# Kernel tuning notes

Measured on AMD Instinct MI355X. Metric: run time of the kernel, lower is better.

## Reference

```python
import jax, jax.numpy as jnp
import numpy as np

N = 200000   # nodes
R = 4        # relations
E = 1000000  # edges per relation
B = 1024     # graphs in batch


def _graph_conv(h, s, d, ew, W, b):
    """DGL GraphConv, norm='both', optional edge_weight. h:[N,F_in] -> [N,F_out]."""
    n = h.shape[0]
    ones = jnp.ones(s.shape[0], dtype=h.dtype)
    out_deg = jnp.clip(jax.ops.segment_sum(ones, s, num_segments=n), 1.0)
    in_deg = jnp.clip(jax.ops.segment_sum(ones, d, num_segments=n), 1.0)
    hs = h * jax.lax.rsqrt(out_deg)[:, None]          # src-side norm
    m = hs[s]                                         # gather: [E, F_in]
    if ew is not None:
        m = m * ew[:, None]
    agg = jax.ops.segment_sum(m, d, num_segments=n)   # scatter-sum: [N, F_in]
    rst = agg * jax.lax.rsqrt(in_deg)[:, None]        # dst-side norm
    return rst @ W + b


def _hetero_layer(h, src, dst, ew, W, b):
    out = None
    for r in range(R):
        ewr = None if ew is None else ew[r]
        o = _graph_conv(h, src[r], dst[r], ewr, W[r], b[r])
        out = o if out is None else out + o
    return out


def setup_inputs() -> dict:
    key = jax.random.key(0)
    ks = jax.random.split(key, 10)
    feat = jax.random.normal(ks[0], (N, 2), dtype=jnp.float32)
    src = jax.random.randint(ks[1], (R, E), 0, N, dtype=jnp.int32)
    dst = jax.random.randint(ks[2], (R, E), 0, N, dtype=jnp.int32)
    ew = jax.random.uniform(ks[3], (R, E), dtype=jnp.float32)
    graph_ids = jnp.sort(jax.random.randint(ks[4], (N,), 0, B, dtype=jnp.int32))
    W1 = jax.random.normal(ks[5], (R, 2, 16), dtype=jnp.float32) * 0.5
    b1 = jnp.zeros((R, 16), dtype=jnp.float32)
    W2 = jax.random.normal(ks[6], (R, 16, 16), dtype=jnp.float32) * 0.25
    b2 = jnp.zeros((R, 16), dtype=jnp.float32)
    Wc = jax.random.normal(ks[7], (16, 2), dtype=jnp.float32) * 0.25
    bc = jnp.zeros((2,), dtype=jnp.float32)
    return {"feat": feat, "src": src, "dst": dst, "ew": ew,
            "graph_ids": graph_ids, "W1": W1, "b1": b1,
            "W2": W2, "b2": b2, "Wc": Wc, "bc": bc}


def reference(feat, src, dst, ew, graph_ids, W1, b1, W2, b2, Wc, bc):
    # layer 1: per-relation weighted GraphConv, summed over relations
    h = _hetero_layer(feat, src, dst, ew, W1, b1)
    h = jax.nn.relu(h)
    # layer 2: no edge weights (kwargs not forwarded in original code)
    h = _hetero_layer(h, src, dst, None, W2, b2)
    # mean_nodes per graph in the batch
    sums = jax.ops.segment_sum(h, graph_ids, num_segments=B)          # [B,16]
    cnts = jax.ops.segment_sum(jnp.ones((N,), h.dtype), graph_ids, num_segments=B)
    hg = sums / jnp.clip(cnts, 1.0)[:, None]
    return hg @ Wc + bc                                               # [B,2]
```

## Files before the change

### kernel.cpp

```cpp
#include <hip/hip_runtime.h>
#include <hip/hip_fp16.h>

#define NN 200000
#define RR 4
#define EE 1000000
#define BB 1024
#define RN (RR*NN)

#define BSH 7
#define BSZ 128
#define NB 1563
#define RK (RR*NB)
#define EPB 16384
#define SBT 1024
#define BPR ((EE + EPB - 1) / EPB)
#define GSLOTS 32
#define CAPB 1024

#define SRC_OF(u)  (((u) >> 7) & 0x3FFFF)
#define DL_OF(u)   ((int)((u) & 127))
#define DEG_OF(u)  ((u) >> 25)

#define OFF_POOL   0
#define OFF_CNT    (OFF_POOL + BB*16)
#define OFF_GCUR_S (OFF_CNT + BB)
#define OFF_GCUR_D (OFF_GCUR_S + RK)
#define ZERO_UNITS (OFF_GCUR_D + RK)
#define OFF_DEGB   ZERO_UNITS
#define OFF_INVI   (OFF_DEGB + RN/4)
#define OFF_RW16   (OFF_INVI + RN)
#define OFF_AGG1   (OFF_RW16 + RN/2)
#define OFF_H1H    (OFF_AGG1 + RN*2)
#define OFF_KW_    (OFF_H1H + NN*8)
#define OFF_KW     (OFF_KW_ + (OFF_KW_ & 1))


__global__ __launch_bounds__(SBT) void k_scat_src(const int* __restrict__ src,
                                                  int* __restrict__ gcur_s,
                                                  unsigned char* __restrict__ srcbin) {
  __shared__ int cnt[NB];
  __shared__ int base[NB];
  __shared__ int lcur[NB];
  int t = threadIdx.x, r = blockIdx.y, c0 = blockIdx.x * EPB;
  for (int i = t; i < NB; i += SBT) cnt[i] = 0;
  __syncthreads();
  for (int i = t; i < EPB; i += SBT) {
    int e = c0 + i;
    if (e < EE) atomicAdd(&cnt[src[r * EE + e] >> BSH], 1);
  }
  __syncthreads();
  for (int b = t; b < NB; b += SBT) {
    int v = cnt[b];
    base[b] = v ? atomicAdd(&gcur_s[r * NB + b], v) : 0;
    lcur[b] = 0;
  }
  __syncthreads();
  for (int i = t; i < EPB; i += SBT) {
    int e = c0 + i;
    if (e < EE) {
      int s = src[r * EE + e];
      int b = s >> BSH;
      int off = base[b] + atomicAdd(&lcur[b], 1);
      if (off < CAPB)
        srcbin[(size_t)(r * NB + b) * CAPB + off] = (unsigned char)(s & (BSZ - 1));
    }
  }
}

__global__ __launch_bounds__(128) void k_deg(const unsigned char* __restrict__ srcbin,
                                             const int* __restrict__ gcur_s,
                                             unsigned char* __restrict__ degb) {
  __shared__ int cnt[BSZ];
  int t = threadIdx.x, b = blockIdx.x, r = blockIdx.y;
  cnt[t] = 0;
  __syncthreads();
  int k = r * NB + b;
  size_t st = (size_t)k * CAPB;
  int m = min(gcur_s[k], CAPB);
  for (int e = t; e < m; e += 128) atomicAdd(&cnt[srcbin[st + e]], 1);
  __syncthreads();
  int n = (b << BSH) + t;
  if (n < NN) degb[r * NN + n] = (unsigned char)min(max(cnt[t], 1), 63);
}

__global__ __launch_bounds__(SBT) void k_scat_dst(const int* __restrict__ src,
                                                  const int* __restrict__ dst,
                                                  const float* __restrict__ ew,
                                                  const unsigned char* __restrict__ degb,
                                                  int* __restrict__ gcur_d,
                                                  long long* __restrict__ kw) {
  __shared__ int cnt[NB];
  __shared__ int base[NB];
  __shared__ int lcur[NB];
  int t = threadIdx.x, r = blockIdx.y, c0 = blockIdx.x * EPB;
  for (int i = t; i < NB; i += SBT) cnt[i] = 0;
  __syncthreads();
  for (int i = t; i < EPB; i += SBT) {
    int e = c0 + i;
    if (e < EE) atomicAdd(&cnt[dst[r * EE + e] >> BSH], 1);
  }
  __syncthreads();
  for (int b = t; b < NB; b += SBT) {
    int v = cnt[b];
    base[b] = v ? atomicAdd(&gcur_d[r * NB + b], v) : 0;
    lcur[b] = 0;
  }
  __syncthreads();
  for (int i = t; i < EPB; i += SBT) {
    int e = c0 + i;
    if (e < EE) {
      int idx = r * EE + e;
      int d = dst[idx], s = src[idx];
      int b = d >> BSH;
      int off = base[b] + atomicAdd(&lcur[b], 1);
      if (off < CAPB) {
        unsigned dg = degb[r * NN + s];
        float io = rsqrtf((float)dg);
        unsigned short w1h = __half_as_ushort(__float2half_rn(ew[idx] * io));
        unsigned low = (unsigned)(d & (BSZ - 1)) | ((unsigned)s << 7) | (dg << 25);
        kw[(size_t)(r * NB + b) * CAPB + off] =
            (long long)(((unsigned long long)w1h << 32) | low);
      }
    }
  }
}

__global__ __launch_bounds__(256) void k_l1a(long long* __restrict__ kw,
                                             const int* __restrict__ gcur_d,
                                             const float* __restrict__ feat,
                                             float* __restrict__ invi,
                                             unsigned short* __restrict__ rw16,
                                             float* __restrict__ agg1) {
  __shared__ long long bufraw[CAPB];
  __shared__ long long bufsort[CAPB];
  __shared__ int cnt[BSZ];
  __shared__ int scn[BSZ];
  __shared__ int cur[BSZ];
  __shared__ float la[BSZ * 3];
  int t = threadIdx.x, b = blockIdx.x, r = blockIdx.y;
  int n0 = b << BSH;
  int k = r * NB + b;
  size_t st = (size_t)k * CAPB;
  int m = min(gcur_d[k], CAPB);
  if (t < BSZ) { cnt[t] = 0; la[t * 3] = 0.f; la[t * 3 + 1] = 0.f; }
  for (int i = t; i < m; i += 256) bufraw[i] = kw[st + i];
  __syncthreads();
  for (int i = t; i < m; i += 256)
    atomicAdd(&cnt[DL_OF((unsigned)bufraw[i])], 1);
  __syncthreads();
  if (t < BSZ) scn[t] = cnt[t];
  __syncthreads();
  for (int off = 1; off < BSZ; off <<= 1) {
    int v = (t < BSZ && t >= off) ? scn[t - off] : 0;
    __syncthreads();
    if (t < BSZ) scn[t] += v;
    __syncthreads();
  }
  if (t < BSZ) {
    int excl = scn[t] - cnt[t];
    cur[t] = excl;
    int n = n0 + t;
    if (n < NN) {
      invi[r * NN + n] = rsqrtf((float)max(cnt[t], 1));
      rw16[r * NN + n] = (unsigned short)excl;
    }
  }
  __syncthreads();
  for (int i = t; i < m; i += 256) {
    long long kv = bufraw[i];
    bufsort[atomicAdd(&cur[DL_OF((unsigned)kv)], 1)] = kv;
  }
  __syncthreads();
  {
    unsigned* up = (unsigned*)kw + 2 * st + CAPB;
    for (int i = t; i < m; i += 256) up[i] = (unsigned)bufsort[i];
  }
  {
    int f = t & 1, grp = t >> 1;
    int seg = (m + BSZ - 1) >> 7;
    int e = grp * seg;
    int e1 = min(e + seg, m);
    float acc = 0.f;
    int dlprev = -1, dlfirst = -1;
    for (; e < e1; e++) {
      long long kv = bufsort[e];
      unsigned low = (unsigned)kv;
      int dl = DL_OF(low);
      int s = SRC_OF(low);
      float w = __half2float(__ushort_as_half((unsigned short)((unsigned long long)kv >> 32)));
      float fv = feat[s * 2 + f];
      if (dl != dlprev) {
        if (dlprev < 0) dlfirst = dl;
        else if (dlprev == dlfirst) atomicAdd(&la[dlprev * 3 + f], acc);
        else la[dlprev * 3 + f] = acc;
        acc = 0.f; dlprev = dl;
      }
      acc += fv * w;
    }
    if (dlprev >= 0) atomicAdd(&la[dlprev * 3 + f], acc);
  }
  __syncthreads();
  if (t < BSZ) {
    int n = n0 + t;
    if (n < NN)
      ((float2*)agg1)[r * NN + n] = make_float2(la[t * 3], la[t * 3 + 1]);
  }
}

__device__ __forceinline__ unsigned pack2h(float a, float b) {
  __half2 h = __floats2half2_rn(a, b);
  return *reinterpret_cast<unsigned*>(&h);
}

__global__ __launch_bounds__(256) void k_l1b(const float* __restrict__ agg1,
                                             const float* __restrict__ invi,
                                             const float* __restrict__ W1,
                                             const float* __restrict__ b1,
                                             __half* __restrict__ h1h) {
  __shared__ float sW[RR * 2 * 16];
  __shared__ float sb[16];
  int t = threadIdx.x, b = blockIdx.x;
  if (t < RR * 2 * 16) sW[t] = W1[t];
  if (t < 16) {
    float s = 0.f;
    for (int r = 0; r < RR; r++) s += b1[r * 16 + t];
    sb[t] = s;
  }
  __syncthreads();
  int n = b * 256 + t;
  if (n >= NN) return;
  float acc[16];
#pragma unroll
  for (int j = 0; j < 16; j++) acc[j] = sb[j];
#pragma unroll
  for (int r = 0; r < RR; r++) {
    float iv = invi[r * NN + n];
    float2 a = ((const float2*)agg1)[r * NN + n];
    float a0 = a.x * iv, a1 = a.y * iv;
#pragma unroll
    for (int j = 0; j < 16; j++)
      acc[j] += a0 * sW[(r * 2 + 0) * 16 + j] + a1 * sW[(r * 2 + 1) * 16 + j];
  }
#pragma unroll
  for (int j = 0; j < 16; j++) acc[j] = fmaxf(acc[j], 0.f);
  uint4 u0, u1;
  u0.x = pack2h(acc[0], acc[1]);  u0.y = pack2h(acc[2], acc[3]);
  u0.z = pack2h(acc[4], acc[5]);  u0.w = pack2h(acc[6], acc[7]);
  u1.x = pack2h(acc[8], acc[9]);  u1.y = pack2h(acc[10], acc[11]);
  u1.z = pack2h(acc[12], acc[13]); u1.w = pack2h(acc[14], acc[15]);
  uint4* o = (uint4*)(h1h + (size_t)n * 16);
  o[0] = u0; o[1] = u1;
}

__device__ __forceinline__ void acc8(float* acc, uint4 u, float w) {
  float2 p;
  p = __half22float2(*(__half2*)&u.x); acc[0] += p.x * w; acc[1] += p.y * w;
  p = __half22float2(*(__half2*)&u.y); acc[2] += p.x * w; acc[3] += p.y * w;
  p = __half22float2(*(__half2*)&u.z); acc[4] += p.x * w; acc[5] += p.y * w;
  p = __half22float2(*(__half2*)&u.w); acc[6] += p.x * w; acc[7] += p.y * w;
}

__global__ __launch_bounds__(256) void k_l2(const long long* __restrict__ kw,
                                            const int* __restrict__ gcur_d,
                                            const unsigned short* __restrict__ rw16,
                                            const __half* __restrict__ h1h,
                                            const float* __restrict__ invi,
                                            const float* __restrict__ W2,
                                            const int* __restrict__ gid,
                                            float* __restrict__ pool,
                                            float* __restrict__ cnt) {
  __shared__ float agg[BSZ * 17];
  __shared__ float sW[16 * 16];
  __shared__ int   sg[BSZ];
  __shared__ unsigned short srw[BSZ + 1];
  __shared__ float gslot[GSLOTS * 16];
  __shared__ int   cslot[GSLOTS];
  __shared__ int   present[GSLOTS];
  int t = threadIdx.x, b = blockIdx.x, r = blockIdx.y;
  int n0 = b << BSH;
  int k = r * NB + b;
  int m = min(gcur_d[k], CAPB);
  sW[t] = W2[r * 256 + t];
  if (t < GSLOTS) { cslot[t] = 0; present[t] = 0; }
  for (int i = t; i < GSLOTS * 16; i += 256) gslot[i] = 0.f;
  if (t < BSZ) {
    int n = n0 + t;
    srw[t] = (n < NN) ? rw16[r * NN + n] : (unsigned short)m;
  }
  if (t == BSZ) srw[BSZ] = (unsigned short)m;
  __syncthreads();
  const uint4* h4p = (const uint4*)h1h;
  const unsigned* rb = (const unsigned*)kw + 2 * (size_t)k * CAPB + CAPB;
  int f8 = t & 1, g = t >> 1;
  int e = srw[g], en = srw[g + 1];
  float acc[8];
#pragma unroll
  for (int j = 0; j < 8; j++) acc[j] = 0.f;
  for (; e + 3 < en; e += 4) {
    unsigned r0 = rb[e], r1 = rb[e + 1], r2 = rb[e + 2], r3 = rb[e + 3];
    uint4 u0 = h4p[(size_t)SRC_OF(r0) * 2 + f8];
    uint4 u1 = h4p[(size_t)SRC_OF(r1) * 2 + f8];
    uint4 u2 = h4p[(size_t)SRC_OF(r2) * 2 + f8];
    uint4 u3 = h4p[(size_t)SRC_OF(r3) * 2 + f8];
    acc8(acc, u0, rsqrtf((float)DEG_OF(r0)));
    acc8(acc, u1, rsqrtf((float)DEG_OF(r1)));
    acc8(acc, u2, rsqrtf((float)DEG_OF(r2)));
    acc8(acc, u3, rsqrtf((float)DEG_OF(r3)));
  }
  for (; e < en; e++) {
    unsigned rr = rb[e];
    uint4 u = h4p[(size_t)SRC_OF(rr) * 2 + f8];
    acc8(acc, u, rsqrtf((float)DEG_OF(rr)));
  }
#pragma unroll
  for (int j = 0; j < 8; j++) agg[g * 17 + 8 * f8 + j] = acc[j];
  __syncthreads();
  int n = n0 + t;
  int g0 = gid[n0];
  bool valid = (t < BSZ) && (n < NN);
  float out[16];
#pragma unroll
  for (int j = 0; j < 16; j++) out[j] = 0.f;
  if (valid) {
    float iv = invi[r * NN + n];
#pragma unroll
    for (int kk = 0; kk < 16; kk++) {
      float a = agg[t * 17 + kk] * iv;
#pragma unroll
      for (int j = 0; j < 16; j++) out[j] += a * sW[kk * 16 + j];
    }
  }
  __syncthreads();
  if (t < BSZ) {
    sg[t] = valid ? (gid[n] - g0) : -1;
#pragma unroll
    for (int j = 0; j < 16; j++) agg[t * 17 + j] = out[j];
  }
  __syncthreads();
  {
    int f = t & 15, i0 = t >> 4;
    for (int i = i0; i < BSZ; i += 16) {
      int gsN = sg[i];
      if (gsN < 0) continue;
      float v = agg[i * 17 + f];
      if (gsN < GSLOTS) {
        atomicAdd(&gslot[gsN * 16 + f], v);
        if (f == 0) {
          present[gsN] = 1;
          if (r == 0) atomicAdd(&cslot[gsN], 1);
        }
      } else {
        atomicAdd(&pool[(g0 + gsN) * 16 + f], v);
        if (f == 0 && r == 0) atomicAdd(&cnt[g0 + gsN], 1.0f);
      }
    }
  }
  __syncthreads();
  if (t < GSLOTS * 16) {
    int gsN = t >> 4, f = t & 15;
    if (present[gsN]) atomicAdd(&pool[(g0 + gsN) * 16 + f], gslot[t]);
  }
  if (r == 0 && t < GSLOTS && cslot[t] > 0)
    atomicAdd(&cnt[g0 + t], (float)cslot[t]);
}

__global__ __launch_bounds__(256) void k_final(const float* __restrict__ pool,
                                               const float* __restrict__ cnt,
                                               const float* __restrict__ b2,
                                               const float* __restrict__ Wc,
                                               const float* __restrict__ bc,
                                               float* __restrict__ out) {
  int b = blockIdx.x * 256 + threadIdx.x;
  if (b >= BB) return;
  float c = cnt[b];
  float inv = 1.0f / fmaxf(c, 1.0f);
  float o0 = bc[0], o1 = bc[1];
#pragma unroll
  for (int j = 0; j < 16; j++) {
    float sb = 0.f;
    for (int r = 0; r < RR; r++) sb += b2[r * 16 + j];
    float v = (pool[b * 16 + j] + c * sb) * inv;
    o0 += v * Wc[j * 2 + 0];
    o1 += v * Wc[j * 2 + 1];
  }
  out[b * 2 + 0] = o0;
  out[b * 2 + 1] = o1;
}

extern "C" void kernel_launch(void* const* d_in, const int* in_sizes, int n_in,
                              void* d_out, int out_size, void* d_ws, size_t ws_size,
                              hipStream_t stream) {
  const float* feat = (const float*)d_in[0];
  const int*   src  = (const int*)d_in[1];
  const int*   dst  = (const int*)d_in[2];
  const float* ew   = (const float*)d_in[3];
  const int*   gid  = (const int*)d_in[4];
  const float* W1   = (const float*)d_in[5];
  const float* b1   = (const float*)d_in[6];
  const float* W2   = (const float*)d_in[7];
  const float* b2   = (const float*)d_in[8];
  const float* Wc   = (const float*)d_in[9];
  const float* bc   = (const float*)d_in[10];

  char* ws = (char*)d_ws;
  float* pool   = (float*)(ws + (size_t)OFF_POOL   * 4);
  float* cnt    = (float*)(ws + (size_t)OFF_CNT    * 4);
  int*   gcur_s = (int*)  (ws + (size_t)OFF_GCUR_S * 4);
  int*   gcur_d = (int*)  (ws + (size_t)OFF_GCUR_D * 4);
  unsigned char*  degb = (unsigned char*) (ws + (size_t)OFF_DEGB * 4);
  float* invi   = (float*)(ws + (size_t)OFF_INVI   * 4);
  unsigned short* rw16 = (unsigned short*)(ws + (size_t)OFF_RW16 * 4);
  float* agg1   = (float*)(ws + (size_t)OFF_AGG1   * 4);
  __half* h1h   = (__half*)(ws + (size_t)OFF_H1H   * 4);
  long long* kw = (long long*)(ws + (size_t)OFF_KW * 4);

  hipMemsetAsync(d_ws, 0, (size_t)ZERO_UNITS * 4, stream);

  k_scat_src<<<dim3(BPR, RR), SBT, 0, stream>>>(src, gcur_s, (unsigned char*)kw);
  k_deg     <<<dim3(NB, RR), 128, 0, stream>>>((const unsigned char*)kw, gcur_s, degb);
  k_scat_dst<<<dim3(BPR, RR), SBT, 0, stream>>>(src, dst, ew, degb, gcur_d, kw);
  k_l1a     <<<dim3(NB, RR), 256, 0, stream>>>(kw, gcur_d, feat, invi, rw16, agg1);
  k_l1b     <<<(NN + 255) / 256, 256, 0, stream>>>(agg1, invi, W1, b1, h1h);
  k_l2      <<<dim3(NB, RR), 256, 0, stream>>>(kw, gcur_d, rw16, h1h, invi, W2, gid, pool, cnt);
  k_final   <<<(BB + 255) / 256, 256, 0, stream>>>(pool, cnt, b2, Wc, bc, (float*)d_out);
}
```

Baseline: 338.4 us.

## Replace per-128-node dst binning with two-pass superbin scatter and sort

The destination scatter now bins edges into 2048-node superbins (98 per relation) instead of 1563 small bins, and a new k_sortB kernel counting-sorts each superbin by node into compact src/weight arrays. k_l1a and k_l2 then read their edge ranges from these sorted arrays using per-node offsets. This cuts the number of global atomic bin cursors and shared-memory histogram work in the scatter pass, and gives more coalesced bin writes. The cost is an extra kernel and an extra pass over the edge data. Superbin capacity is fixed, and offsets are stored as 16-bit values, so overflow is possible on skewed inputs.

Result: slower. 370.7 us (+9.5%).

```diff
diff --git a/kernel.cpp b/kernel.cpp
--- a/kernel.cpp
+++ b/kernel.cpp
@@ -11,9 +11,12 @@
 #define BSZ 128
 #define NB 1563
 #define RK (RR*NB)
+#define SBSH 11
+#define NSB 98
+#define CAPSB 11264
 #define EPB 16384
+#define BPR ((EE + EPB - 1) / EPB)
 #define SBT 1024
-#define BPR ((EE + EPB - 1) / EPB)
 #define GSLOTS 32
 #define CAPB 1024
 
@@ -21,18 +24,19 @@
 #define DL_OF(u)   ((int)((u) & 127))
 #define DEG_OF(u)  ((u) >> 25)
 
-#define OFF_POOL   0
-#define OFF_CNT    (OFF_POOL + BB*16)
-#define OFF_GCUR_S (OFF_CNT + BB)
-#define OFF_GCUR_D (OFF_GCUR_S + RK)
-#define ZERO_UNITS (OFF_GCUR_D + RK)
-#define OFF_DEGB   ZERO_UNITS
-#define OFF_INVI   (OFF_DEGB + RN/4)
-#define OFF_RW16   (OFF_INVI + RN)
-#define OFF_AGG1   (OFF_RW16 + RN/2)
-#define OFF_H1H    (OFF_AGG1 + RN*2)
-#define OFF_KW_    (OFF_H1H + NN*8)
-#define OFF_KW     (OFF_KW_ + (OFF_KW_ & 1))
+#define OFF_POOL    0
+#define OFF_CNT     (OFF_POOL + BB*16)
+#define OFF_GCUR_S  (OFF_CNT + BB)
+#define OFF_GCUR_SB (OFF_GCUR_S + RK)
+#define ZERO_UNITS  (OFF_GCUR_SB + RR*NSB)
+#define OFF_DEGB    ZERO_UNITS
+#define OFF_INVI    (OFF_DEGB + RN/4)
+#define OFF_RW16    (OFF_INVI + RN)
+#define OFF_AGG1    (OFF_RW16 + RN/2)
+#define OFF_H1H     (OFF_AGG1 + RN*2)
+#define OFF_SBB     (OFF_H1H + NN*8)
+#define OFF_CS      (OFF_SBB + RR*NSB*CAPSB*2)
+#define OFF_W1S     (OFF_CS + RR*NSB*CAPSB)
 
 
 __global__ __launch_bounds__(SBT) void k_scat_src(const int* __restrict__ src,
@@ -83,27 +87,27 @@
   if (n < NN) degb[r * NN + n] = (unsigned char)min(max(cnt[t], 1), 63);
 }
 
-__global__ __launch_bounds__(SBT) void k_scat_dst(const int* __restrict__ src,
+__global__ __launch_bounds__(SBT) void k_scat_sbA(const int* __restrict__ src,
                                                   const int* __restrict__ dst,
                                                   const float* __restrict__ ew,
                                                   const unsigned char* __restrict__ degb,
-                                                  int* __restrict__ gcur_d,
-                                                  long long* __restrict__ kw) {
-  __shared__ int cnt[NB];
-  __shared__ int base[NB];
-  __shared__ int lcur[NB];
+                                                  int* __restrict__ gcur_sb,
+                                                  long long* __restrict__ sbb) {
+  __shared__ int cnt[NSB];
+  __shared__ int base[NSB];
+  __shared__ int lcur[NSB];
   int t = threadIdx.x, r = blockIdx.y, c0 = blockIdx.x * EPB;
-  for (int i = t; i < NB; i += SBT) cnt[i] = 0;
+  if (t < NSB) cnt[t] = 0;
   __syncthreads();
   for (int i = t; i < EPB; i += SBT) {
     int e = c0 + i;
-    if (e < EE) atomicAdd(&cnt[dst[r * EE + e] >> BSH], 1);
-  }
-  __syncthreads();
-  for (int b = t; b < NB; b += SBT) {
-    int v = cnt[b];
-    base[b] = v ? atomicAdd(&gcur_d[r * NB + b], v) : 0;
-    lcur[b] = 0;
+    if (e < EE) atomicAdd(&cnt[dst[r * EE + e] >> SBSH], 1);
+  }
+  __syncthreads();
+  if (t < NSB) {
+    int v = cnt[t];
+    base[t] = v ? atomicAdd(&gcur_sb[r * NSB + t], v) : 0;
+    lcur[t] = 0;
   }
   __syncthreads();
   for (int i = t; i < EPB; i += SBT) {
@@ -111,83 +115,108 @@
     if (e < EE) {
       int idx = r * EE + e;
       int d = dst[idx], s = src[idx];
-      int b = d >> BSH;
-      int off = base[b] + atomicAdd(&lcur[b], 1);
-      if (off < CAPB) {
+      int sb = d >> SBSH;
+      int off = base[sb] + atomicAdd(&lcur[sb], 1);
+      if (off < CAPSB) {
         unsigned dg = degb[r * NN + s];
         float io = rsqrtf((float)dg);
         unsigned short w1h = __half_as_ushort(__float2half_rn(ew[idx] * io));
+        unsigned bl = (unsigned)(d >> BSH) & 15;
         unsigned low = (unsigned)(d & (BSZ - 1)) | ((unsigned)s << 7) | (dg << 25);
-        kw[(size_t)(r * NB + b) * CAPB + off] =
-            (long long)(((unsigned long long)w1h << 32) | low);
+        unsigned high = (unsigned)w1h | (bl << 16);
+        sbb[(size_t)(r * NSB + sb) * CAPSB + off] =
+            (long long)(((unsigned long long)high << 32) | low);
       }
     }
   }
 }
 
-__global__ __launch_bounds__(256) void k_l1a(long long* __restrict__ kw,
-                                             const int* __restrict__ gcur_d,
+__global__ __launch_bounds__(1024) void k_sortB(const long long* __restrict__ sbb,
+                                                const int* __restrict__ gcur_sb,
+                                                float* __restrict__ invi,
+                                                unsigned short* __restrict__ rw16,
+                                                unsigned* __restrict__ cs,
+                                                unsigned short* __restrict__ w1s) {
+  __shared__ int cnt2[2048];
+  __shared__ int cur2[2048];
+  __shared__ int ssum[1024];
+  int t = threadIdx.x, sb = blockIdx.x, r = blockIdx.y;
+  int ksb = r * NSB + sb;
+  size_t sbase = (size_t)ksb * CAPSB;
+  int m = min(gcur_sb[ksb], CAPSB);
+  cnt2[t] = 0; cnt2[t + 1024] = 0;
+  __syncthreads();
+  for (int i = t; i < m; i += 1024) {
+    long long kv = sbb[sbase + i];
+    int node = (((int)(kv >> 48) & 15) << BSH) | ((int)kv & (BSZ - 1));
+    atomicAdd(&cnt2[node], 1);
+  }
+  __syncthreads();
+  int a0 = cnt2[2 * t], a1 = cnt2[2 * t + 1];
+  ssum[t] = a0 + a1;
+  __syncthreads();
+  for (int off = 1; off < 1024; off <<= 1) {
+    int v = (t >= off) ? ssum[t - off] : 0;
+    __syncthreads();
+    ssum[t] += v;
+    __syncthreads();
+  }
+  int e0 = (t > 0) ? ssum[t - 1] : 0;
+  int e1 = e0 + a0;
+  cur2[2 * t] = e0;
+  cur2[2 * t + 1] = e1;
+  {
+    int nbase = (sb << SBSH) + 2 * t;
+    if (nbase < NN) {
+      rw16[r * NN + nbase] = (unsigned short)e0;
+      invi[r * NN + nbase] = rsqrtf((float)max(a0, 1));
+    }
+    if (nbase + 1 < NN) {
+      rw16[r * NN + nbase + 1] = (unsigned short)e1;
+      invi[r * NN + nbase + 1] = rsqrtf((float)max(a1, 1));
+    }
+  }
+  __syncthreads();
+  for (int i = t; i < m; i += 1024) {
+    long long kv = sbb[sbase + i];
+    unsigned low = (unsigned)kv;
+    int node = (((int)(kv >> 48) & 15) << BSH) | (int)(low & (BSZ - 1));
+    int pos = atomicAdd(&cur2[node], 1);
+    cs[sbase + pos] = low;
+    w1s[sbase + pos] = (unsigned short)((unsigned long long)kv >> 32);
+  }
+}
+
+__global__ __launch_bounds__(256) void k_l1a(const unsigned* __restrict__ cs,
+                                             const unsigned short* __restrict__ w1s,
+                                             const int* __restrict__ gcur_sb,
+                                             const unsigned short* __restrict__ rw16,
                                              const float* __restrict__ feat,
-                                             float* __restrict__ invi,
-                                             unsigned short* __restrict__ rw16,
                                              float* __restrict__ agg1) {
-  __shared__ long long bufraw[CAPB];
-  __shared__ long long bufsort[CAPB];
-  __shared__ int cnt[BSZ];
-  __shared__ int scn[BSZ];
-  __shared__ int cur[BSZ];
   __shared__ float la[BSZ * 3];
   int t = threadIdx.x, b = blockIdx.x, r = blockIdx.y;
   int n0 = b << BSH;
-  int k = r * NB + b;
-  size_t st = (size_t)k * CAPB;
-  int m = min(gcur_d[k], CAPB);
-  if (t < BSZ) { cnt[t] = 0; la[t * 3] = 0.f; la[t * 3 + 1] = 0.f; }
-  for (int i = t; i < m; i += 256) bufraw[i] = kw[st + i];
-  __syncthreads();
-  for (int i = t; i < m; i += 256)
-    atomicAdd(&cnt[DL_OF((unsigned)bufraw[i])], 1);
-  __syncthreads();
-  if (t < BSZ) scn[t] = cnt[t];
-  __syncthreads();
-  for (int off = 1; off < BSZ; off <<= 1) {
-    int v = (t < BSZ && t >= off) ? scn[t - off] : 0;
-    __syncthreads();
-    if (t < BSZ) scn[t] += v;
-    __syncthreads();
-  }
-  if (t < BSZ) {
-    int excl = scn[t] - cnt[t];
-    cur[t] = excl;
-    int n = n0 + t;
-    if (n < NN) {
-      invi[r * NN + n] = rsqrtf((float)max(cnt[t], 1));
-      rw16[r * NN + n] = (unsigned short)excl;
-    }
-  }
-  __syncthreads();
-  for (int i = t; i < m; i += 256) {
-    long long kv = bufraw[i];
-    bufsort[atomicAdd(&cur[DL_OF((unsigned)kv)], 1)] = kv;
-  }
-  __syncthreads();
-  {
-    unsigned* up = (unsigned*)kw + 2 * st + CAPB;
-    for (int i = t; i < m; i += 256) up[i] = (unsigned)bufsort[i];
-  }
+  int sb = b >> 4, bl = b & 15;
+  int ksb = r * NSB + sb;
+  size_t sbase = (size_t)ksb * CAPSB;
+  int m_sb = min(gcur_sb[ksb], CAPSB);
+  int stB = rw16[r * NN + n0];
+  int enB = (bl == 15 || n0 + BSZ >= NN) ? m_sb : (int)rw16[r * NN + n0 + BSZ];
+  if (t < BSZ) { la[t * 3] = 0.f; la[t * 3 + 1] = 0.f; }
+  __syncthreads();
   {
     int f = t & 1, grp = t >> 1;
-    int seg = (m + BSZ - 1) >> 7;
-    int e = grp * seg;
-    int e1 = min(e + seg, m);
+    int len = enB - stB;
+    int seg = (len + BSZ - 1) >> 7;
+    int e = stB + grp * seg;
+    int e1 = min(e + seg, enB);
     float acc = 0.f;
     int dlprev = -1, dlfirst = -1;
     for (; e < e1; e++) {
-      long long kv = bufsort[e];
-      unsigned low = (unsigned)kv;
+      unsigned low = cs[sbase + e];
       int dl = DL_OF(low);
       int s = SRC_OF(low);
-      float w = __half2float(__ushort_as_half((unsigned short)((unsigned long long)kv >> 32)));
+      float w = __half2float(__ushort_as_half(w1s[sbase + e]));
       float fv = feat[s * 2 + f];
       if (dl != dlprev) {
         if (dlprev < 0) dlfirst = dl;
@@ -260,8 +289,8 @@
   p = __half22float2(*(__half2*)&u.w); acc[6] += p.x * w; acc[7] += p.y * w;
 }
 
-__global__ __launch_bounds__(256) void k_l2(const long long* __restrict__ kw,
-                                            const int* __restrict__ gcur_d,
+__global__ __launch_bounds__(256) void k_l2(const unsigned* __restrict__ cs,
+                                            const int* __restrict__ gcur_sb,
                                             const unsigned short* __restrict__ rw16,
                                             const __half* __restrict__ h1h,
                                             const float* __restrict__ invi,
@@ -278,19 +307,23 @@
   __shared__ int   present[GSLOTS];
   int t = threadIdx.x, b = blockIdx.x, r = blockIdx.y;
   int n0 = b << BSH;
-  int k = r * NB + b;
-  int m = min(gcur_d[k], CAPB);
+  int sb = b >> 4, bl = b & 15;
+  int ksb = r * NSB + sb;
+  size_t sbase = (size_t)ksb * CAPSB;
+  int m_sb = min(gcur_sb[ksb], CAPSB);
   sW[t] = W2[r * 256 + t];
   if (t < GSLOTS) { cslot[t] = 0; present[t] = 0; }
   for (int i = t; i < GSLOTS * 16; i += 256) gslot[i] = 0.f;
   if (t < BSZ) {
     int n = n0 + t;
-    srw[t] = (n < NN) ? rw16[r * NN + n] : (unsigned short)m;
-  }
-  if (t == BSZ) srw[BSZ] = (unsigned short)m;
+    srw[t] = (n < NN) ? rw16[r * NN + n] : (unsigned short)m_sb;
+  }
+  if (t == BSZ)
+    srw[BSZ] = (bl == 15 || n0 + BSZ >= NN) ? (unsigned short)m_sb
+                                            : rw16[r * NN + n0 + BSZ];
   __syncthreads();
   const uint4* h4p = (const uint4*)h1h;
-  const unsigned* rb = (const unsigned*)kw + 2 * (size_t)k * CAPB + CAPB;
+  const unsigned* rb = cs + sbase;
   int f8 = t & 1, g = t >> 1;
   int e = srw[g], en = srw[g + 1];
   float acc[8];
@@ -403,24 +436,27 @@
   const float* bc   = (const float*)d_in[10];
 
   char* ws = (char*)d_ws;
-  float* pool   = (float*)(ws + (size_t)OFF_POOL   * 4);
-  float* cnt    = (float*)(ws + (size_t)OFF_CNT    * 4);
-  int*   gcur_s = (int*)  (ws + (size_t)OFF_GCUR_S * 4);
-  int*   gcur_d = (int*)  (ws + (size_t)OFF_GCUR_D * 4);
+  float* pool    = (float*)(ws + (size_t)OFF_POOL    * 4);
+  float* cnt     = (float*)(ws + (size_t)OFF_CNT     * 4);
+  int*   gcur_s  = (int*)  (ws + (size_t)OFF_GCUR_S  * 4);
+  int*   gcur_sb = (int*)  (ws + (size_t)OFF_GCUR_SB * 4);
   unsigned char*  degb = (unsigned char*) (ws + (size_t)OFF_DEGB * 4);
-  float* invi   = (float*)(ws + (size_t)OFF_INVI   * 4);
+  float* invi    = (float*)(ws + (size_t)OFF_INVI    * 4);
   unsigned short* rw16 = (unsigned short*)(ws + (size_t)OFF_RW16 * 4);
-  float* agg1   = (float*)(ws + (size_t)OFF_AGG1   * 4);
-  __half* h1h   = (__half*)(ws + (size_t)OFF_H1H   * 4);
-  long long* kw = (long long*)(ws + (size_t)OFF_KW * 4);
+  float* agg1    = (float*)(ws + (size_t)OFF_AGG1    * 4);
+  __half* h1h    = (__half*)(ws + (size_t)OFF_H1H    * 4);
+  long long* sbb = (long long*)(ws + (size_t)OFF_SBB * 4);
+  unsigned* cs   = (unsigned*)(ws + (size_t)OFF_CS   * 4);
+  unsigned short* w1s = (unsigned short*)(ws + (size_t)OFF_W1S * 4);
 
   hipMemsetAsync(d_ws, 0, (size_t)ZERO_UNITS * 4, stream);
 
-  k_scat_src<<<dim3(BPR, RR), SBT, 0, stream>>>(src, gcur_s, (unsigned char*)kw);
-  k_deg     <<<dim3(NB, RR), 128, 0, stream>>>((const unsigned char*)kw, gcur_s, degb);
-  k_scat_dst<<<dim3(BPR, RR), SBT, 0, stream>>>(src, dst, ew, degb, gcur_d, kw);
-  k_l1a     <<<dim3(NB, RR), 256, 0, stream>>>(kw, gcur_d, feat, invi, rw16, agg1);
+  k_scat_src<<<dim3(BPR, RR), SBT, 0, stream>>>(src, gcur_s, (unsigned char*)sbb);
+  k_deg     <<<dim3(NB, RR), 128, 0, stream>>>((const unsigned char*)sbb, gcur_s, degb);
+  k_scat_sbA<<<dim3(BPR, RR), SBT, 0, stream>>>(src, dst, ew, degb, gcur_sb, sbb);
+  k_sortB   <<<dim3(NSB, RR), 1024, 0, stream>>>(sbb, gcur_sb, invi, rw16, cs, w1s);
+  k_l1a     <<<dim3(NB, RR), 256, 0, stream>>>(cs, w1s, gcur_sb, rw16, feat, agg1);
   k_l1b     <<<(NN + 255) / 256, 256, 0, stream>>>(agg1, invi, W1, b1, h1h);
-  k_l2      <<<dim3(NB, RR), 256, 0, stream>>>(kw, gcur_d, rw16, h1h, invi, W2, gid, pool, cnt);
+  k_l2      <<<dim3(NB, RR), 256, 0, stream>>>(cs, gcur_sb, rw16, h1h, invi, W2, gid, pool, cnt);
   k_final   <<<(BB + 255) / 256, 256, 0, stream>>>(pool, cnt, b2, Wc, bc, (float*)d_out);
 }
```
